# Optimization experiments

Hardware: AMD Instinct MI355X
Metric: run time of the kernel (lower is better)

## Reference

```python
import jax, jax.numpy as jnp
import numpy as np

N, C, T, V = 64, 64, 256, 25
S, OC = 3, 64
IC = OC // 2  # inter_channels
BN_EPS = 1e-5


def setup_inputs() -> dict:
    key = jax.random.key(0)
    ks = jax.random.split(key, 8)
    return {
        "x": jax.random.normal(ks[0], (N, C, T, V), dtype=jnp.float32),
        "A": jax.random.normal(ks[1], (S, V, V), dtype=jnp.float32),
        "Wa": jax.random.normal(ks[2], (S, IC, C), dtype=jnp.float32) * 0.05,
        "ba": jax.random.normal(ks[3], (S, IC), dtype=jnp.float32) * 0.05,
        "Wb": jax.random.normal(ks[4], (S, IC, C), dtype=jnp.float32) * 0.05,
        "bb": jax.random.normal(ks[5], (S, IC), dtype=jnp.float32) * 0.05,
        "Wd": jax.random.normal(ks[6], (S, OC, C), dtype=jnp.float32) * 0.05,
        "bd": jax.random.normal(ks[7], (S, OC), dtype=jnp.float32) * 0.05,
        "bn_gamma": jnp.ones((OC,), dtype=jnp.float32),
        "bn_beta": jnp.zeros((OC,), dtype=jnp.float32),
    }


def reference(x, A, Wa, ba, Wb, bb, Wd, bd, bn_gamma, bn_beta):
    n, c, t, v = x.shape
    s, ic = Wa.shape[0], Wa.shape[1]
    # 1x1 convs over all subsets at once: [N,S,IC,T,V]
    a = jnp.einsum('nctv,sic->nsitv', x, Wa) + ba[None, :, :, None, None]
    b = jnp.einsum('nctv,sic->nsitv', x, Wb) + bb[None, :, :, None, None]
    # A1: permute(0,3,1,2).view(N,V,IC*T) per subset -> [N,S,V,IC*T]
    A1 = a.transpose(0, 1, 4, 2, 3).reshape(n, s, v, ic * t)
    # A2: view(N,IC*T,V) per subset -> [N,S,IC*T,V]
    A2 = b.reshape(n, s, ic * t, v)
    scores = jnp.einsum('nsvk,nskw->nsvw', A1, A2) / (ic * t)
    # torch Softmax(-2): normalize over the first V axis (rows of [V,V])
    att = jax.nn.softmax(scores, axis=-2) + A[None]  # [N,S,V,V]
    # x.view(N,C*T,V) @ att  ->  contract over source joint v
    z = jnp.einsum('nctv,nsvw->nsctw', x, att)  # [N,S,C,T,V]
    # conv_d per subset then sum over subsets (the y accumulation)
    y = jnp.einsum('nsctw,soc->notw', z, Wd) + bd.sum(0)[None, :, None, None]
    # BatchNorm2d in inference mode with running_mean=0, running_var=1
    y = bn_gamma[None, :, None, None] * y * (1.0 / jnp.sqrt(1.0 + BN_EPS)) + bn_beta[None, :, None, None]
    # residual=False -> residual(x) == 0; self.relu is defined but never applied
    return y
```

## Files before the change

kernel.cpp:

```cpp
#include <hip/hip_runtime.h>


#define NCHUNK    16
#define ATT_OFF   0
#define ATT_SZ    (64*3*25*32)
#define PART_OFF  153600
#define PART_SZ   (64*NCHUNK*3*625)
#define WAT_OFF   (PART_OFF + PART_SZ)
#define WBT_OFF   (WAT_OFF + 3*64*32)
#define WDT_OFF   (WBT_OFF + 3*64*32)
#define ALPHA_OFF (WDT_OFF + 3*64*64)
#define BETA_OFF  (ALPHA_OFF + 64)

__global__ __launch_bounds__(256) void k0_prep(
    float* __restrict__ wsf,
    const float* __restrict__ Wa, const float* __restrict__ Wb,
    const float* __restrict__ Wd, const float* __restrict__ bd,
    const float* __restrict__ gamma, const float* __restrict__ beta)
{
  int idx = blockIdx.x * 256 + threadIdx.x;
  if (idx < 6144) {
    int s = idx / 2048, r = idx - s * 2048, c = r >> 5, i = r & 31;
    wsf[WAT_OFF + idx] = Wa[s * 2048 + i * 64 + c];
    wsf[WBT_OFF + idx] = Wb[s * 2048 + i * 64 + c];
  }
  if (idx < 12288) {
    int s = idx / 4096, r = idx - s * 4096, c = r >> 6, o = r & 63;
    wsf[WDT_OFF + idx] = Wd[s * 4096 + o * 64 + c];
  }
  if (idx < 64) {
    float al = gamma[idx] * rsqrtf(1.0f + 1e-5f);
    wsf[ALPHA_OFF + idx] = al;
    float bs = bd[idx] + bd[64 + idx] + bd[128 + idx];
    wsf[BETA_OFF + idx] = beta[idx] + al * bs;
  }
}

__global__ __launch_bounds__(256) void k1_scores(
    const float* __restrict__ x,
    const float* __restrict__ WaT, const float* __restrict__ WbT,
    const float* __restrict__ ba, const float* __restrict__ bb,
    float* __restrict__ part)
{
  const int nb = blockIdx.x;
  const int n = nb >> 4;
  const int ch = nb & 15;
  const int tid = threadIdx.x;
  const int wave = tid >> 6;
  const int lane = tid & 63;
  const int tgrp = wave >> 1;
  const int i0 = __builtin_amdgcn_readfirstlane((wave & 1) << 4);
  const int tl = tgrp * 2 + lane / 25;
  const int tlc = tl < 4 ? tl : 3;
  const int v = lane % 25;
  const bool act = lane < 50;
  const int tlv = tgrp * 50 + lane;

  __shared__ float ab[6400];
  __shared__ float red[1875];
  float* const red2 = ab;

  const int tp = tid % 25;
  const int ks = tid / 25;
  const int v5 = (tp / 5) * 5, w5 = (tp % 5) * 5;
  const int kb = (ks < 8) ? ks * 13 : (104 + (ks - 8) * 12);
  const int kcnt = (ks < 8) ? 13 : 12;

  for (int idx = tid; idx < 1875; idx += 256) red[idx] = 0.0f;
  __syncthreads();

  for (int sub = 0; sub < 4; ++sub) {
    const int t0 = ch * 16 + sub * 4;
    for (int s = 0; s < 3; ++s) {
      float fa[16], fb[16];
      #pragma unroll
      for (int j = 0; j < 16; ++j) {
        fa[j] = ba[s * 32 + i0 + j];
        fb[j] = bb[s * 32 + i0 + j];
      }
      const float* xp = x + n * 409600 + (t0 + tlc) * 25 + v;
      const float* wap = WaT + s * 2048 + i0;
      const float* wbp = WbT + s * 2048 + i0;
      for (int c8 = 0; c8 < 64; c8 += 8) {
        float xv[8];
        #pragma unroll
        for (int u = 0; u < 8; ++u)
          xv[u] = act ? xp[(c8 + u) * 6400] : 0.0f;
        #pragma unroll
        for (int u = 0; u < 8; ++u) {
          const float* wa8 = wap + (c8 + u) * 32;
          const float* wb8 = wbp + (c8 + u) * 32;
          #pragma unroll
          for (int j = 0; j < 16; ++j) {
            fa[j] = fmaf(wa8[j], xv[u], fa[j]);
            fb[j] = fmaf(wb8[j], xv[u], fb[j]);
          }
        }
      }
      __syncthreads();
      if (act) {
        #pragma unroll
        for (int j = 0; j < 16; ++j) {
          ab[(i0 + j) * 100 + tlv]        = fa[j];
          ab[3200 + (i0 + j) * 100 + tlv] = fb[j];
        }
      }
      __syncthreads();
      float sc[5][5];
      if (tid < 250) {
        #pragma unroll
        for (int dv = 0; dv < 5; ++dv)
          #pragma unroll
          for (int dw = 0; dw < 5; ++dw) sc[dv][dw] = 0.0f;
        for (int kk = 0; kk < kcnt; ++kk) {
          const int k = kb + kk;
          float av[5], bv[5];
          #pragma unroll
          for (int d = 0; d < 5; ++d) {
            av[d] = ab[k * 25 + v5 + d];
            bv[d] = ab[3200 + k * 25 + w5 + d];
          }
          #pragma unroll
          for (int dv = 0; dv < 5; ++dv)
            #pragma unroll
            for (int dw = 0; dw < 5; ++dw)
              sc[dv][dw] = fmaf(av[dv], bv[dw], sc[dv][dw]);
        }
      }
      __syncthreads();
      if (tid < 250) {
        #pragma unroll
        for (int dv = 0; dv < 5; ++dv)
          #pragma unroll
          for (int dw = 0; dw < 5; ++dw)
            red2[ks * 625 + (v5 + dv) * 25 + (w5 + dw)] = sc[dv][dw];
      }
      __syncthreads();
      {
        float acc0 = 0.0f, acc1 = 0.0f, acc2 = 0.0f;
        #pragma unroll
        for (int q = 0; q < 10; ++q) {
          acc0 += red2[q * 625 + tid];
          acc1 += red2[q * 625 + tid + 256];
          if (tid < 113) acc2 += red2[q * 625 + tid + 512];
        }
        red[s * 625 + tid]        += acc0;
        red[s * 625 + tid + 256]  += acc1;
        if (tid < 113) red[s * 625 + tid + 512] += acc2;
      }
    }
  }
  __syncthreads();
  for (int s = 0; s < 3; ++s)
    for (int idx = tid; idx < 625; idx += 256)
      part[((n * NCHUNK + ch) * 3 + s) * 625 + idx] = red[s * 625 + idx];
}

__global__ __launch_bounds__(64) void k2_softmax(
    const float* __restrict__ part, const float* __restrict__ A,
    float* __restrict__ att)
{
  const int ns = blockIdx.x;
  const int n = ns / 3, s = ns % 3;
  const int w = threadIdx.x;
  float* ap = att + ns * 800;
  if (w < 25) {
    float sc[25];
    float m = -3.0e38f;
    #pragma unroll
    for (int v = 0; v < 25; ++v) {
      float acc = 0.0f;
      for (int chk = 0; chk < NCHUNK; ++chk)
        acc += part[((n * NCHUNK + chk) * 3 + s) * 625 + v * 25 + w];
      sc[v] = acc * (1.0f / 8192.0f);
      m = fmaxf(m, sc[v]);
    }
    float sum = 0.0f;
    #pragma unroll
    for (int v = 0; v < 25; ++v) { sc[v] = expf(sc[v] - m); sum += sc[v]; }
    const float inv = 1.0f / sum;
    #pragma unroll
    for (int v = 0; v < 25; ++v)
      ap[v * 32 + w] = sc[v] * inv + A[(s * 25 + v) * 25 + w];
  } else if (w < 32) {
    for (int v = 0; v < 25; ++v) ap[v * 32 + w] = 0.0f;
  }
}

__global__ __launch_bounds__(256) void k3_out(
    const float* __restrict__ x, const float* __restrict__ att,
    const float* __restrict__ WdT,
    const float* __restrict__ alpha, const float* __restrict__ betaE,
    float* __restrict__ out)
{
  const int nb = blockIdx.x;
  const int n = nb >> 7;
  const int t0 = (nb & 127) * 2;
  const int tid = threadIdx.x;
  const int wave = tid >> 6;
  const int lane = tid & 63;

  __shared__ float xs[3200];
  __shared__ float zt[4224];

  const float* xg = x + n * 409600 + t0 * 25;
  for (int idx = tid; idx < 3200; idx += 256) {
    int c = idx / 50, p = idx - c * 50;
    xs[idx] = xg[c * 6400 + p];
  }

  const int c0A = __builtin_amdgcn_readfirstlane((wave & 1) << 5);
  const int w0A = __builtin_amdgcn_readfirstlane((wave >> 1) << 4);
  const int o0B = __builtin_amdgcn_readfirstlane(wave << 4);
  const int tB = lane >> 5, wB = lane & 31;
  const int xbase = c0A * 50 + lane * 25;
  const int zwb   = c0A * 66 + lane * 33 + w0A;
  const int zrb   = tB * 33 + wB;

  float yacc[16];
  #pragma unroll
  for (int j = 0; j < 16; ++j) yacc[j] = 0.0f;

  __syncthreads();
  for (int s = 0; s < 3; ++s) {
    const float* attp = att + (n * 3 + s) * 800 + w0A;
    float za[16];
    #pragma unroll
    for (int j = 0; j < 16; ++j) za[j] = 0.0f;
    #pragma unroll 5
    for (int v = 0; v < 25; ++v) {
      float xv = xs[xbase + v];
      #pragma unroll
      for (int j = 0; j < 16; ++j)
        za[j] = fmaf(attp[v * 32 + j], xv, za[j]);
    }
    #pragma unroll
    for (int j = 0; j < 16; ++j) zt[zwb + j] = za[j];
    __syncthreads();
    const float* wdp = WdT + s * 4096 + o0B;
    #pragma unroll 4
    for (int c = 0; c < 64; ++c) {
      float zv = zt[c * 66 + zrb];
      #pragma unroll
      for (int j = 0; j < 16; ++j)
        yacc[j] = fmaf(wdp[c * 64 + j], zv, yacc[j]);
    }
    __syncthreads();
  }
  if (wB < 25) {
    const int t = t0 + tB;
    float* op = out + n * 409600 + t * 25 + wB;
    #pragma unroll
    for (int j = 0; j < 16; ++j) {
      const int o = o0B + j;
      op[o * 6400] = alpha[o] * yacc[j] + betaE[o];
    }
  }
}

extern "C" void kernel_launch(void* const* d_in, const int* in_sizes, int n_in,
                              void* d_out, int out_size, void* d_ws, size_t ws_size,
                              hipStream_t stream) {
  const float* x     = (const float*)d_in[0];
  const float* A     = (const float*)d_in[1];
  const float* Wa    = (const float*)d_in[2];
  const float* ba    = (const float*)d_in[3];
  const float* Wb    = (const float*)d_in[4];
  const float* bb    = (const float*)d_in[5];
  const float* Wd    = (const float*)d_in[6];
  const float* bd    = (const float*)d_in[7];
  const float* gamma = (const float*)d_in[8];
  const float* beta  = (const float*)d_in[9];
  float* wsf = (float*)d_ws;
  float* out = (float*)d_out;

  k0_prep<<<64, 256, 0, stream>>>(wsf, Wa, Wb, Wd, bd, gamma, beta);
  k1_scores<<<1024, 256, 0, stream>>>(x, wsf + WAT_OFF, wsf + WBT_OFF,
                                      ba, bb, wsf + PART_OFF);
  k2_softmax<<<192, 64, 0, stream>>>(wsf + PART_OFF, A, wsf + ATT_OFF);
  k3_out<<<8192, 256, 0, stream>>>(x, wsf + ATT_OFF, wsf + WDT_OFF,
                                   wsf + ALPHA_OFF, wsf + BETA_OFF, out);
}
```

Before: 571.2 us.

## Split score kernel into more time chunks and parallelize chunk reduction

```diff
diff --git a/kernel.cpp b/kernel.cpp
--- a/kernel.cpp
+++ b/kernel.cpp
@@ -1,11 +1,11 @@
 #include <hip/hip_runtime.h>
 
 
-#define NCHUNK    16
+#define NCH       64
 #define ATT_OFF   0
 #define ATT_SZ    (64*3*25*32)
 #define PART_OFF  153600
-#define PART_SZ   (64*NCHUNK*3*625)
+#define PART_SZ   (64*NCH*3*625)
 #define WAT_OFF   (PART_OFF + PART_SZ)
 #define WBT_OFF   (WAT_OFF + 3*64*32)
 #define WDT_OFF   (WBT_OFF + 3*64*32)
@@ -36,15 +36,15 @@
   }
 }
 
-__global__ __launch_bounds__(256) void k1_scores(
+__global__ __launch_bounds__(256, 6) void k1_scores(
     const float* __restrict__ x,
     const float* __restrict__ WaT, const float* __restrict__ WbT,
     const float* __restrict__ ba, const float* __restrict__ bb,
     float* __restrict__ part)
 {
   const int nb = blockIdx.x;
-  const int n = nb >> 4;
-  const int ch = nb & 15;
+  const int n = nb >> 6;
+  const int ch = nb & 63;
   const int tid = threadIdx.x;
   const int wave = tid >> 6;
   const int lane = tid & 63;
@@ -54,10 +54,8 @@
   const int tlc = tl < 4 ? tl : 3;
   const int v = lane % 25;
   const bool act = lane < 50;
-  const int tlv = tgrp * 50 + lane;
-
-  __shared__ float ab[6400];
-  __shared__ float red[1875];
+
+  __shared__ float ab[6656];
   float* const red2 = ab;
 
   const int tp = tid % 25;
@@ -66,122 +64,119 @@
   const int kb = (ks < 8) ? ks * 13 : (104 + (ks - 8) * 12);
   const int kcnt = (ks < 8) ? 13 : 12;
 
-  for (int idx = tid; idx < 1875; idx += 256) red[idx] = 0.0f;
-  __syncthreads();
-
-  for (int sub = 0; sub < 4; ++sub) {
-    const int t0 = ch * 16 + sub * 4;
-    for (int s = 0; s < 3; ++s) {
-      float fa[16], fb[16];
+  const int t0 = ch * 4;
+  const float* xp = x + n * 409600 + (t0 + tlc) * 25 + v;
+
+  #pragma unroll 1
+  for (int s = 0; s < 3; ++s) {
+    float fa[16], fb[16];
+    #pragma unroll
+    for (int j = 0; j < 16; ++j) {
+      fa[j] = ba[s * 32 + i0 + j];
+      fb[j] = bb[s * 32 + i0 + j];
+    }
+    const float* wap = WaT + s * 2048 + i0;
+    const float* wbp = WbT + s * 2048 + i0;
+    for (int c8 = 0; c8 < 64; c8 += 8) {
+      float xv[8];
+      #pragma unroll
+      for (int u = 0; u < 8; ++u)
+        xv[u] = act ? xp[(c8 + u) * 6400] : 0.0f;
+      #pragma unroll
+      for (int u = 0; u < 8; ++u) {
+        const float* wa8 = wap + (c8 + u) * 32;
+        const float* wb8 = wbp + (c8 + u) * 32;
+        #pragma unroll
+        for (int j = 0; j < 16; ++j) {
+          fa[j] = fmaf(wa8[j], xv[u], fa[j]);
+          fb[j] = fmaf(wb8[j], xv[u], fb[j]);
+        }
+      }
+    }
+    __syncthreads();
+    if (act) {
       #pragma unroll
       for (int j = 0; j < 16; ++j) {
-        fa[j] = ba[s * 32 + i0 + j];
-        fb[j] = bb[s * 32 + i0 + j];
-      }
-      const float* xp = x + n * 409600 + (t0 + tlc) * 25 + v;
-      const float* wap = WaT + s * 2048 + i0;
-      const float* wbp = WbT + s * 2048 + i0;
-      for (int c8 = 0; c8 < 64; c8 += 8) {
-        float xv[8];
-        #pragma unroll
-        for (int u = 0; u < 8; ++u)
-          xv[u] = act ? xp[(c8 + u) * 6400] : 0.0f;
-        #pragma unroll
-        for (int u = 0; u < 8; ++u) {
-          const float* wa8 = wap + (c8 + u) * 32;
-          const float* wb8 = wbp + (c8 + u) * 32;
-          #pragma unroll
-          for (int j = 0; j < 16; ++j) {
-            fa[j] = fmaf(wa8[j], xv[u], fa[j]);
-            fb[j] = fmaf(wb8[j], xv[u], fb[j]);
-          }
+        ab[(i0 + j) * 104 + tl * 26 + v]        = fa[j];
+        ab[3328 + (i0 + j) * 104 + tl * 26 + v] = fb[j];
+      }
+    }
+    __syncthreads();
+    float sc[5][5];
+    if (tid < 250) {
+      #pragma unroll
+      for (int dv = 0; dv < 5; ++dv)
+        #pragma unroll
+        for (int dw = 0; dw < 5; ++dw) sc[dv][dw] = 0.0f;
+      for (int kk = 0; kk < kcnt; ++kk) {
+        const int k = kb + kk;
+        float av[5], bv[5];
+        #pragma unroll
+        for (int d = 0; d < 5; ++d) {
+          av[d] = ab[k * 26 + v5 + d];
+          bv[d] = ab[3328 + k * 26 + w5 + d];
         }
-      }
-      __syncthreads();
-      if (act) {
-        #pragma unroll
-        for (int j = 0; j < 16; ++j) {
-          ab[(i0 + j) * 100 + tlv]        = fa[j];
-          ab[3200 + (i0 + j) * 100 + tlv] = fb[j];
-        }
-      }
-      __syncthreads();
-      float sc[5][5];
-      if (tid < 250) {
-        #pragma unroll
-        for (int dv = 0; dv < 5; ++dv)
-          #pragma unroll
-          for (int dw = 0; dw < 5; ++dw) sc[dv][dw] = 0.0f;
-        for (int kk = 0; kk < kcnt; ++kk) {
-          const int k = kb + kk;
-          float av[5], bv[5];
-          #pragma unroll
-          for (int d = 0; d < 5; ++d) {
-            av[d] = ab[k * 25 + v5 + d];
-            bv[d] = ab[3200 + k * 25 + w5 + d];
-          }
-          #pragma unroll
-          for (int dv = 0; dv < 5; ++dv)
-            #pragma unroll
-            for (int dw = 0; dw < 5; ++dw)
-              sc[dv][dw] = fmaf(av[dv], bv[dw], sc[dv][dw]);
-        }
-      }
-      __syncthreads();
-      if (tid < 250) {
         #pragma unroll
         for (int dv = 0; dv < 5; ++dv)
           #pragma unroll
           for (int dw = 0; dw < 5; ++dw)
-            red2[ks * 625 + (v5 + dv) * 25 + (w5 + dw)] = sc[dv][dw];
-      }
-      __syncthreads();
-      {
-        float acc0 = 0.0f, acc1 = 0.0f, acc2 = 0.0f;
-        #pragma unroll
-        for (int q = 0; q < 10; ++q) {
-          acc0 += red2[q * 625 + tid];
-          acc1 += red2[q * 625 + tid + 256];
-          if (tid < 113) acc2 += red2[q * 625 + tid + 512];
-        }
-        red[s * 625 + tid]        += acc0;
-        red[s * 625 + tid + 256]  += acc1;
-        if (tid < 113) red[s * 625 + tid + 512] += acc2;
-      }
-    }
-  }
-  __syncthreads();
-  for (int s = 0; s < 3; ++s)
-    for (int idx = tid; idx < 625; idx += 256)
-      part[((n * NCHUNK + ch) * 3 + s) * 625 + idx] = red[s * 625 + idx];
-}
-
-__global__ __launch_bounds__(64) void k2_softmax(
+            sc[dv][dw] = fmaf(av[dv], bv[dw], sc[dv][dw]);
+      }
+    }
+    __syncthreads();
+    if (tid < 250) {
+      #pragma unroll
+      for (int dv = 0; dv < 5; ++dv)
+        #pragma unroll
+        for (int dw = 0; dw < 5; ++dw)
+          red2[ks * 632 + (v5 + dv) * 25 + (w5 + dw)] = sc[dv][dw];
+    }
+    __syncthreads();
+    {
+      float acc0 = 0.0f, acc1 = 0.0f, acc2 = 0.0f;
+      #pragma unroll
+      for (int q = 0; q < 10; ++q) {
+        acc0 += red2[q * 632 + tid];
+        acc1 += red2[q * 632 + tid + 256];
+        if (tid < 113) acc2 += red2[q * 632 + tid + 512];
+      }
+      float* pp = part + ((n * NCH + ch) * 3 + s) * 625;
+      pp[tid]       = acc0;
+      pp[tid + 256] = acc1;
+      if (tid < 113) pp[tid + 512] = acc2;
+    }
+  }
+}
+
+__global__ __launch_bounds__(256) void k2_softmax(
     const float* __restrict__ part, const float* __restrict__ A,
     float* __restrict__ att)
 {
   const int ns = blockIdx.x;
   const int n = ns / 3, s = ns % 3;
-  const int w = threadIdx.x;
+  const int tid = threadIdx.x;
+  __shared__ float sm[625];
+  for (int idx = tid; idx < 625; idx += 256) {
+    float acc = 0.0f;
+    #pragma unroll 8
+    for (int chk = 0; chk < NCH; ++chk)
+      acc += part[((n * NCH + chk) * 3 + s) * 625 + idx];
+    sm[idx] = acc * (1.0f / 8192.0f);
+  }
+  __syncthreads();
   float* ap = att + ns * 800;
+  const int w = tid;
   if (w < 25) {
-    float sc[25];
     float m = -3.0e38f;
     #pragma unroll
-    for (int v = 0; v < 25; ++v) {
-      float acc = 0.0f;
-      for (int chk = 0; chk < NCHUNK; ++chk)
-        acc += part[((n * NCHUNK + chk) * 3 + s) * 625 + v * 25 + w];
-      sc[v] = acc * (1.0f / 8192.0f);
-      m = fmaxf(m, sc[v]);
-    }
-    float sum = 0.0f;
-    #pragma unroll
-    for (int v = 0; v < 25; ++v) { sc[v] = expf(sc[v] - m); sum += sc[v]; }
+    for (int v = 0; v < 25; ++v) m = fmaxf(m, sm[v * 25 + w]);
+    float e[25], sum = 0.0f;
+    #pragma unroll
+    for (int v = 0; v < 25; ++v) { e[v] = expf(sm[v * 25 + w] - m); sum += e[v]; }
     const float inv = 1.0f / sum;
     #pragma unroll
     for (int v = 0; v < 25; ++v)
-      ap[v * 32 + w] = sc[v] * inv + A[(s * 25 + v) * 25 + w];
+      ap[v * 32 + w] = e[v] * inv + A[(s * 25 + v) * 25 + w];
   } else if (w < 32) {
     for (int v = 0; v < 25; ++v) ap[v * 32 + w] = 0.0f;
   }
@@ -222,6 +217,7 @@
   for (int j = 0; j < 16; ++j) yacc[j] = 0.0f;
 
   __syncthreads();
+  #pragma unroll 1
   for (int s = 0; s < 3; ++s) {
     const float* attp = att + (n * 3 + s) * 800 + w0A;
     float za[16];
@@ -275,9 +271,9 @@
   float* out = (float*)d_out;
 
   k0_prep<<<64, 256, 0, stream>>>(wsf, Wa, Wb, Wd, bd, gamma, beta);
-  k1_scores<<<1024, 256, 0, stream>>>(x, wsf + WAT_OFF, wsf + WBT_OFF,
+  k1_scores<<<4096, 256, 0, stream>>>(x, wsf + WAT_OFF, wsf + WBT_OFF,
                                       ba, bb, wsf + PART_OFF);
-  k2_softmax<<<192, 64, 0, stream>>>(wsf + PART_OFF, A, wsf + ATT_OFF);
+  k2_softmax<<<192, 256, 0, stream>>>(wsf + PART_OFF, A, wsf + ATT_OFF);
   k3_out<<<8192, 256, 0, stream>>>(x, wsf + ATT_OFF, wsf + WDT_OFF,
                                    wsf + ALPHA_OFF, wsf + BETA_OFF, out);
 }
```

Result: slower. 679.5 us (+19.0%).
